# Performance work log

Measured on AMD Instinct MI355X. Metric: run time of the kernel, lower is better.

## Reference

```python
import jax, jax.numpy as jnp
import numpy as np

jax.config.update("jax_enable_x64", True)  # needed for faithful int64 topology hash (31**i weights)

B, SEQ, HID, OUT = 64, 2048, 1024, 1024
MAX_DEPTH = 3
MAX_NODES = 2 ** MAX_DEPTH - 1          # 7
MAX_LEAVES = 2 ** (MAX_DEPTH - 1)       # 4 leaf slots (nodes 3..6)
MAX_SHAPE_IDS = 256


def _gelu(x):
    return jax.nn.gelu(x, approximate=False)  # torch nn.GELU default = exact erf


def setup_inputs() -> dict:
    key = jax.random.key(0)
    ks = jax.random.split(key, 8)
    states = jax.random.normal(ks[0], (B, SEQ, HID), dtype=jnp.float32)

    rng = np.random.default_rng(0)
    lengths = rng.integers(SEQ // 2, SEQ, size=(B,)).astype(np.int64)
    # sorted segment boundaries within [0, lengths), first boundary at 0
    fr = np.sort(rng.random((B, MAX_LEAVES - 1)), axis=1)
    boundaries = np.concatenate(
        [np.zeros((B, 1), np.int64), np.floor(fr * lengths[:, None]).astype(np.int64)], axis=1)
    mask = np.arange(SEQ)[None, :] < lengths[:, None]
    # complete binary tree, depth 3: node 0 root, nodes 1-2 internal, 3-6 leaves
    leaf_order = np.tile(np.arange(MAX_NODES // 2, MAX_NODES, dtype=np.int64), (B, 1))
    active = np.ones((B, MAX_NODES), bool)
    is_leaf = np.concatenate([np.zeros((B, 3), bool), np.ones((B, 4), bool)], axis=1)
    left_child = np.array([1, 3, 5, -1, -1, -1, -1], np.int64)
    right_child = np.array([2, 4, 6, -1, -1, -1, -1], np.int64)
    depth = np.array([0, 1, 1, 2, 2, 2, 2], np.int64)

    def lin(k, fan_in, shape):
        return jax.random.normal(k, shape, dtype=jnp.float32) / np.sqrt(fan_in).astype(np.float32)

    W1 = lin(ks[1], HID, (HID, OUT)); b1 = jnp.zeros((OUT,), jnp.float32)
    W2 = lin(ks[2], OUT, (OUT, OUT)); b2 = jnp.zeros((OUT,), jnp.float32)
    Wm1 = lin(ks[3], 2 * OUT, (2 * OUT, OUT)); bm1 = jnp.zeros((OUT,), jnp.float32)
    Wm2 = lin(ks[4], OUT, (OUT, OUT)); bm2 = jnp.zeros((OUT,), jnp.float32)
    depth_embed = jax.random.normal(ks[5], (MAX_DEPTH, OUT), dtype=jnp.float32) * 0.02
    shape_embed = jax.random.normal(ks[6], (MAX_SHAPE_IDS, OUT), dtype=jnp.float32) * 0.02

    return dict(
        states=states, mask=jnp.asarray(mask), lengths=jnp.asarray(lengths),
        boundaries=jnp.asarray(boundaries), leaf_order=jnp.asarray(leaf_order),
        active=jnp.asarray(active), is_leaf=jnp.asarray(is_leaf),
        left_child=jnp.asarray(left_child), right_child=jnp.asarray(right_child),
        depth=jnp.asarray(depth),
        W1=W1, b1=b1, W2=W2, b2=b2, Wm1=Wm1, bm1=bm1, Wm2=Wm2, bm2=bm2,
        depth_embed=depth_embed, shape_embed=shape_embed)


def _forward(states, W1, b1, W2, b2, Wm1, bm1, Wm2, bm2, depth_embed, shape_embed,
             mask, lengths, boundaries, leaf_order, active, is_leaf,
             left_child, right_child, depth):
    b, seq, _ = states.shape
    S = boundaries.shape[1]
    max_nodes = left_child.shape[0]

    # ---- 1. vectorized ragged masked segment-mean pooling ----
    pos = jnp.arange(seq)
    # segment id per token: number of boundaries <= t, minus 1
    seg_id = (pos[None, None, :] >= boundaries[:, :, None]).sum(1) - 1      # (b, seq)
    valid = mask & (pos[None, :] < lengths[:, None]) & (seg_id >= 0)
    onehot = ((seg_id[:, :, None] == jnp.arange(S)[None, None, :])
              & valid[:, :, None]).astype(states.dtype)                     # (b, seq, S)
    cnt = onehot.sum(1)                                                     # (b, S)
    pooled = jnp.einsum('bts,bth->bsh', onehot, states) / jnp.clip(cnt, 1.0)[..., None]

    # ---- 2. encode segments + depth embedding, scatter to leaf slots ----
    enc = _gelu(pooled @ W1 + b1) @ W2 + b2                                 # (b, S, D)
    nidx = leaf_order                                                       # (b, S)
    nclip = jnp.maximum(nidx, 0)
    enc = enc + depth_embed[depth[nclip]]
    leaf_ok = (nidx >= 0) & jnp.take_along_axis(is_leaf, nclip, axis=1) & (cnt > 0)
    contrib = enc * leaf_ok[..., None].astype(enc.dtype)
    node_repr = jnp.zeros((b, max_nodes, enc.shape[-1]), enc.dtype)
    node_repr = node_repr.at[jnp.arange(b)[:, None], nclip].add(contrib)

    # ---- 3. bottom-up binary tree merge (loop over fixed small node count) ----
    for i in range(max_nodes - 1, -1, -1):
        lc = left_child[i]
        rc = right_child[i]
        is_int = active[:, i] & ~is_leaf[:, i]                              # (b,)
        l = jnp.take(node_repr, jnp.maximum(lc, 0), axis=1)                 # (b, D)
        r = jnp.take(node_repr, jnp.maximum(rc, 0), axis=1)
        merged = (_gelu(jnp.concatenate([l, r], axis=-1) @ Wm1 + bm1) @ Wm2 + bm2
                  + depth_embed[depth[i]])
        upd = is_int.any() & (lc != -1)
        newv = jnp.where(upd, merged * is_int[:, None].astype(merged.dtype),
                         node_repr[:, i])
        node_repr = node_repr.at[:, i].set(newv)

    # ---- 4. topology hash -> shape embedding ----
    pattern = active.astype(jnp.int64) * 2 + is_leaf.astype(jnp.int64)      # (b, nodes)
    weights = 31 ** jnp.arange(max_nodes, dtype=jnp.int64)
    hashed = (pattern * weights[None, :]).sum(1)
    shape_ids = jnp.abs(hashed) % shape_embed.shape[0]
    return node_repr[:, 0] + shape_embed[shape_ids]


def reference(states, mask, lengths, boundaries, leaf_order, active, is_leaf,
              left_child, right_child, depth,
              W1, b1, W2, b2, Wm1, bm1, Wm2, bm2, depth_embed, shape_embed):
    return _forward(states, W1, b1, W2, b2, Wm1, bm1, Wm2, bm2,
                    depth_embed, shape_embed, mask, lengths, boundaries,
                    leaf_order, active, is_leaf, left_child, right_child, depth)
```

## Files before the change

### kernel.cpp

```cpp
#include <hip/hip_runtime.h>
#include <cstdint>
#include <cstddef>

#define SEQ   2048
#define HID   1024
#define NBAT  64
#define NSEG  4
#define NNODE 7
#define TCHUNK 128

__device__ __forceinline__ float gelu_f(float x) {
  return 0.5f * x * (1.0f + erff(x * 0.7071067811865476f));
}

__global__ __launch_bounds__(256) void pool_kernel(
    const float* __restrict__ states, const int* __restrict__ boundaries,
    const int* __restrict__ lengths, float* __restrict__ pooled_sum)
{
  const int tc = blockIdx.x, b = blockIdx.y;
  const int tid = threadIdx.x;
  const int len = lengths[b];
  int bnd[5];
  bnd[0] = boundaries[b * 4 + 0];
  bnd[1] = boundaries[b * 4 + 1];
  bnd[2] = boundaries[b * 4 + 2];
  bnd[3] = boundaries[b * 4 + 3];
  bnd[4] = len;
  const int clo = tc * TCHUNK, chi = clo + TCHUNK;
  const float4* S = (const float4*)(states + (size_t)b * SEQ * HID);

  #pragma unroll
  for (int s = 0; s < NSEG; ++s) {
    int lo = bnd[s]     > clo ? bnd[s]     : clo;
    int hi = bnd[s + 1] < chi ? bnd[s + 1] : chi;
    if (lo >= hi) continue;
    float4 acc = make_float4(0.f, 0.f, 0.f, 0.f);
    int t = lo;
    for (; t + 4 <= hi; t += 4) {
      float4 v0 = S[(size_t)(t + 0) * (HID / 4) + tid];
      float4 v1 = S[(size_t)(t + 1) * (HID / 4) + tid];
      float4 v2 = S[(size_t)(t + 2) * (HID / 4) + tid];
      float4 v3 = S[(size_t)(t + 3) * (HID / 4) + tid];
      acc.x += (v0.x + v1.x) + (v2.x + v3.x);
      acc.y += (v0.y + v1.y) + (v2.y + v3.y);
      acc.z += (v0.z + v1.z) + (v2.z + v3.z);
      acc.w += (v0.w + v1.w) + (v2.w + v3.w);
    }
    for (; t < hi; ++t) {
      float4 v = S[(size_t)t * (HID / 4) + tid];
      acc.x += v.x; acc.y += v.y; acc.z += v.z; acc.w += v.w;
    }
    float* dst = pooled_sum + (size_t)(b * NSEG + s) * HID + tid * 4;
    atomicAdd(dst + 0, acc.x);
    atomicAdd(dst + 1, acc.y);
    atomicAdd(dst + 2, acc.z);
    atomicAdd(dst + 3, acc.w);
  }
}

#define BM 32
#define BN 64
#define BK 32

template<int AMODE, int SPLIT, int SRCS>
__global__ __launch_bounds__(256) void gemm_kernel(
    const float* __restrict__ A,
    const float* __restrict__ W,
    const float* __restrict__ biasA,
    float* __restrict__ Cp,
    int M, int K,
    const int* __restrict__ boundaries, const int* __restrict__ lengths,
    const int* __restrict__ left_child, const int* __restrict__ right_child,
    const float* __restrict__ node_in, int nodeA, int nodeB)
{
  const int N = 1024;
  __shared__ float As[BK][BM + 2];
  __shared__ float Ws[BK][BN];

  const int tid = threadIdx.x;
  const int n0 = blockIdx.x * BN;
  const int m0 = blockIdx.y * BM;
  const int z  = blockIdx.z;
  const int Kloc = K / SPLIT;
  const int kbeg = z * Kloc;

  const int am = tid >> 3;
  const int ak = (tid & 7) * 4;
  const int wk = tid >> 3;
  const int wn = (tid & 7) * 8;
  const int rm = (tid >> 4) * 2;
  const int cn = (tid & 15) * 4;

  float ainv = 1.0f;
  int lcn = 0, rcn = 0, arow_b = 0;
  if constexpr (AMODE == 1) {
    int m = m0 + am; int b = m >> 2; int s = m & 3;
    int bs = boundaries[b * 4 + s];
    int bn = (s < 3) ? boundaries[b * 4 + s + 1] : lengths[b];
    ainv = 1.0f / fmaxf((float)(bn - bs), 1.0f);
  } else if constexpr (AMODE == 2) {
    int mrow = m0 + am; int mi = mrow >> 6; int b = mrow & 63;
    int node = mi ? nodeB : nodeA;
    lcn = left_child[node]; rcn = right_child[node];
    arow_b = b;
  }

  float acc[2][4] = {{0.f,0.f,0.f,0.f},{0.f,0.f,0.f,0.f}};

  float4 av[SRCS]; float4 bv; float4 wv0, wv1;

  auto issueA = [&](int kcol) {
    if constexpr (AMODE == 3) {
      #pragma unroll
      for (int s = 0; s < SRCS; ++s)
        av[s] = *(const float4*)(A + ((size_t)s * M + (m0 + am)) * (size_t)K + kcol);
      bv = *(const float4*)(biasA + kcol);
    } else if constexpr (AMODE == 2) {
      int child = (kcol < 1024) ? lcn : rcn;
      av[0] = *(const float4*)(node_in + (size_t)(arow_b * NNODE + child) * 1024 + (kcol & 1023));
    } else {
      av[0] = *(const float4*)(A + (size_t)(m0 + am) * K + kcol);
    }
  };

  issueA(kbeg + ak);
  wv0 = *(const float4*)(W + (size_t)(kbeg + wk) * N + n0 + wn);
  wv1 = *(const float4*)(W + (size_t)(kbeg + wk) * N + n0 + wn + 4);

  for (int k0 = 0; k0 < Kloc; k0 += BK) {
    __syncthreads();
    {
      float4 a;
      if constexpr (AMODE == 3) {
        float4 s = av[0];
        #pragma unroll
        for (int q = 1; q < SRCS; ++q) {
          s.x += av[q].x; s.y += av[q].y; s.z += av[q].z; s.w += av[q].w;
        }
        a.x = gelu_f(s.x + bv.x); a.y = gelu_f(s.y + bv.y);
        a.z = gelu_f(s.z + bv.z); a.w = gelu_f(s.w + bv.w);
      } else if constexpr (AMODE == 1) {
        a = av[0];
        a.x *= ainv; a.y *= ainv; a.z *= ainv; a.w *= ainv;
      } else {
        a = av[0];
      }
      As[ak + 0][am] = a.x;
      As[ak + 1][am] = a.y;
      As[ak + 2][am] = a.z;
      As[ak + 3][am] = a.w;
    }
    *(float4*)&Ws[wk][wn]     = wv0;
    *(float4*)&Ws[wk][wn + 4] = wv1;
    __syncthreads();

    const int kn = k0 + BK;
    if (kn < Kloc) {
      issueA(kbeg + kn + ak);
      wv0 = *(const float4*)(W + (size_t)(kbeg + kn + wk) * N + n0 + wn);
      wv1 = *(const float4*)(W + (size_t)(kbeg + kn + wk) * N + n0 + wn + 4);
    }

    #pragma unroll
    for (int kk = 0; kk < BK; ++kk) {
      float2 a2 = *(const float2*)&As[kk][rm];
      float4 w  = *(const float4*)&Ws[kk][cn];
      acc[0][0] += a2.x * w.x; acc[0][1] += a2.x * w.y;
      acc[0][2] += a2.x * w.z; acc[0][3] += a2.x * w.w;
      acc[1][0] += a2.y * w.x; acc[1][1] += a2.y * w.y;
      acc[1][2] += a2.y * w.z; acc[1][3] += a2.y * w.w;
    }
  }

  #pragma unroll
  for (int r = 0; r < 2; ++r) {
    const int m = m0 + rm + r;
    *(float4*)(Cp + ((size_t)z * M + m) * N + n0 + cn) =
        make_float4(acc[r][0], acc[r][1], acc[r][2], acc[r][3]);
  }
}

template<int EPI, int SRCS>
__global__ __launch_bounds__(256) void redepi_kernel(
    const float* __restrict__ P, const float* __restrict__ bias, int M,
    const int* __restrict__ boundaries, const int* __restrict__ lengths,
    const int* __restrict__ leaf_order, const int* __restrict__ active,
    const int* __restrict__ is_leaf, const int* __restrict__ depth,
    const float* __restrict__ dembed, const float* __restrict__ sembed,
    float* __restrict__ node_out, int nodeA, int nodeB)
{
  const int m = blockIdx.x;
  const int n = threadIdx.x * 4;

  float4 x = *(const float4*)(P + (size_t)m * 1024 + n);
  #pragma unroll
  for (int q = 1; q < SRCS; ++q) {
    float4 p = *(const float4*)(P + ((size_t)q * M + m) * 1024 + n);
    x.x += p.x; x.y += p.y; x.z += p.z; x.w += p.w;
  }
  x.x += bias[n + 0]; x.y += bias[n + 1];
  x.z += bias[n + 2]; x.w += bias[n + 3];

  if constexpr (EPI == 1) {
    int b = m >> 2; int s = m & 3;
    int node  = leaf_order[b * 4 + s];
    int nclip = node < 0 ? 0 : node;
    int bs = boundaries[b * 4 + s];
    int bn = (s < 3) ? boundaries[b * 4 + s + 1] : lengths[b];
    bool ok = (node >= 0) && (is_leaf[b * NNODE + nclip] != 0) && (bn - bs > 0);
    int d = depth[nclip];
    const float* de = dembed + (size_t)d * 1024 + n;
    float sc = ok ? 1.0f : 0.0f;
    x.x = (x.x + de[0]) * sc; x.y = (x.y + de[1]) * sc;
    x.z = (x.z + de[2]) * sc; x.w = (x.w + de[3]) * sc;
    *(float4*)(node_out + (size_t)(b * NNODE + nclip) * 1024 + n) = x;
  } else if constexpr (EPI == 2) {
    int mi = m >> 6; int b = m & 63;
    int node = mi ? nodeB : nodeA;
    bool ii = (active[b * NNODE + node] != 0) && (is_leaf[b * NNODE + node] == 0);
    int d = depth[node];
    const float* de = dembed + (size_t)d * 1024 + n;
    float sc = ii ? 1.0f : 0.0f;
    x.x = (x.x + de[0]) * sc; x.y = (x.y + de[1]) * sc;
    x.z = (x.z + de[2]) * sc; x.w = (x.w + de[3]) * sc;
    *(float4*)(node_out + (size_t)(b * NNODE + node) * 1024 + n) = x;
  } else {
    int b = m & 63;
    bool ii = (active[b * NNODE + 0] != 0) && (is_leaf[b * NNODE + 0] == 0);
    int d = depth[0];
    const float* de = dembed + (size_t)d * 1024 + n;
    float sc = ii ? 1.0f : 0.0f;
    long long h = 0, w = 1;
    #pragma unroll
    for (int i = 0; i < NNODE; ++i) {
      long long p = (long long)active[b * NNODE + i] * 2
                  + (long long)is_leaf[b * NNODE + i];
      h += p * w;
      w *= 31;
    }
    long long a = h < 0 ? -h : h;
    int sid = (int)(a % 256);
    const float* se = sembed + (size_t)sid * 1024 + n;
    x.x = (x.x + de[0]) * sc + se[0];
    x.y = (x.y + de[1]) * sc + se[1];
    x.z = (x.z + de[2]) * sc + se[2];
    x.w = (x.w + de[3]) * sc + se[3];
    *(float4*)(node_out + (size_t)b * 1024 + n) = x;
  }
}

extern "C" void kernel_launch(void* const* d_in, const int* in_sizes, int n_in,
                              void* d_out, int out_size, void* d_ws, size_t ws_size,
                              hipStream_t stream)
{
  const float* states     = (const float*)d_in[0];
  const int* lengths      = (const int*)d_in[2];
  const int* boundaries   = (const int*)d_in[3];
  const int* leaf_order   = (const int*)d_in[4];
  const int* active       = (const int*)d_in[5];
  const int* is_leaf      = (const int*)d_in[6];
  const int* left_child   = (const int*)d_in[7];
  const int* right_child  = (const int*)d_in[8];
  const int* depth        = (const int*)d_in[9];
  const float* W1  = (const float*)d_in[10];
  const float* b1  = (const float*)d_in[11];
  const float* W2  = (const float*)d_in[12];
  const float* b2  = (const float*)d_in[13];
  const float* Wm1 = (const float*)d_in[14];
  const float* bm1 = (const float*)d_in[15];
  const float* Wm2 = (const float*)d_in[16];
  const float* bm2 = (const float*)d_in[17];
  const float* dembed = (const float*)d_in[18];
  const float* sembed = (const float*)d_in[19];
  float* out = (float*)d_out;

  float* pooled    = (float*)d_ws;
  float* P1 = pooled + 256 * 1024;
  float* P2 = P1 + 2 * 256 * 1024;
  float* P3 = P2 + 2 * 256 * 1024;
  float* P4 = P3 + 4 * 128 * 1024;
  float* P5 = P4 + 4 * 128 * 1024;
  float* P6 = P5 + 8 * 64 * 1024;
  float* node_repr = P6 + 8 * 64 * 1024;

  hipMemsetAsync(pooled, 0, (size_t)256 * 1024 * sizeof(float), stream);

  pool_kernel<<<dim3(SEQ / TCHUNK, NBAT), 256, 0, stream>>>(
      states, boundaries, lengths, pooled);

  gemm_kernel<1, 2, 1><<<dim3(16, 8, 2), 256, 0, stream>>>(
      pooled, W1, nullptr, P1, 256, 1024,
      boundaries, lengths, nullptr, nullptr, nullptr, -1, -1);

  gemm_kernel<3, 2, 2><<<dim3(16, 8, 2), 256, 0, stream>>>(
      P1, W2, b1, P2, 256, 1024,
      nullptr, nullptr, nullptr, nullptr, nullptr, -1, -1);

  redepi_kernel<1, 2><<<dim3(256), 256, 0, stream>>>(
      P2, b2, 256, boundaries, lengths, leaf_order, active, is_leaf, depth,
      dembed, sembed, node_repr, -1, -1);

  gemm_kernel<2, 4, 1><<<dim3(16, 4, 4), 256, 0, stream>>>(
      nullptr, Wm1, nullptr, P3, 128, 2048,
      nullptr, nullptr, left_child, right_child, node_repr, 1, 2);

  gemm_kernel<3, 4, 4><<<dim3(16, 4, 4), 256, 0, stream>>>(
      P3, Wm2, bm1, P4, 128, 1024,
      nullptr, nullptr, nullptr, nullptr, nullptr, -1, -1);

  redepi_kernel<2, 4><<<dim3(128), 256, 0, stream>>>(
      P4, bm2, 128, boundaries, lengths, leaf_order, active, is_leaf, depth,
      dembed, sembed, node_repr, 1, 2);

  gemm_kernel<2, 8, 1><<<dim3(16, 2, 8), 256, 0, stream>>>(
      nullptr, Wm1, nullptr, P5, 64, 2048,
      nullptr, nullptr, left_child, right_child, node_repr, 0, 0);

  gemm_kernel<3, 8, 8><<<dim3(16, 2, 8), 256, 0, stream>>>(
      P5, Wm2, bm1, P6, 64, 1024,
      nullptr, nullptr, nullptr, nullptr, nullptr, -1, -1);

  redepi_kernel<3, 8><<<dim3(64), 256, 0, stream>>>(
      P6, bm2, 64, boundaries, lengths, leaf_order, active, is_leaf, depth,
      dembed, sembed, out, 0, 0);
}
```

Before: 812.2 us.

## Fuse all stages into one persistent kernel with software grid barriers

Replaces the ten separate launches (pool, six split-K GEMMs, three reduce/epilogue kernels) with a single persistent kernel of 512 blocks that separates stages with atomic-counter grid barriers. The split-K reduction, bias and depth-embedding epilogues are folded into the A-operand load of the next GEMM, which removes the node_repr buffer and the redepi kernels. Split factors are doubled to give 512 blocks per stage. The aim is to remove launch gaps and intermediate round trips. The cost is barrier spin overhead and a deadlock risk if all 512 blocks are not co-resident.

```diff
diff --git a/kernel.cpp b/kernel.cpp
--- a/kernel.cpp
+++ b/kernel.cpp
@@ -2,87 +2,103 @@
 #include <cstdint>
 #include <cstddef>
 
-#define SEQ   2048
-#define HID   1024
-#define NBAT  64
-#define NSEG  4
-#define NNODE 7
+#define SEQ    2048
+#define HID    1024
+#define NBAT   64
+#define NSEG   4
+#define NNODE  7
 #define TCHUNK 128
-
-__device__ __forceinline__ float gelu_f(float x) {
-  return 0.5f * x * (1.0f + erff(x * 0.7071067811865476f));
-}
-
-__global__ __launch_bounds__(256) void pool_kernel(
-    const float* __restrict__ states, const int* __restrict__ boundaries,
-    const int* __restrict__ lengths, float* __restrict__ pooled_sum)
-{
-  const int tc = blockIdx.x, b = blockIdx.y;
-  const int tid = threadIdx.x;
-  const int len = lengths[b];
-  int bnd[5];
-  bnd[0] = boundaries[b * 4 + 0];
-  bnd[1] = boundaries[b * 4 + 1];
-  bnd[2] = boundaries[b * 4 + 2];
-  bnd[3] = boundaries[b * 4 + 3];
-  bnd[4] = len;
-  const int clo = tc * TCHUNK, chi = clo + TCHUNK;
-  const float4* S = (const float4*)(states + (size_t)b * SEQ * HID);
-
-  #pragma unroll
-  for (int s = 0; s < NSEG; ++s) {
-    int lo = bnd[s]     > clo ? bnd[s]     : clo;
-    int hi = bnd[s + 1] < chi ? bnd[s + 1] : chi;
-    if (lo >= hi) continue;
-    float4 acc = make_float4(0.f, 0.f, 0.f, 0.f);
-    int t = lo;
-    for (; t + 4 <= hi; t += 4) {
-      float4 v0 = S[(size_t)(t + 0) * (HID / 4) + tid];
-      float4 v1 = S[(size_t)(t + 1) * (HID / 4) + tid];
-      float4 v2 = S[(size_t)(t + 2) * (HID / 4) + tid];
-      float4 v3 = S[(size_t)(t + 3) * (HID / 4) + tid];
-      acc.x += (v0.x + v1.x) + (v2.x + v3.x);
-      acc.y += (v0.y + v1.y) + (v2.y + v3.y);
-      acc.z += (v0.z + v1.z) + (v2.z + v3.z);
-      acc.w += (v0.w + v1.w) + (v2.w + v3.w);
-    }
-    for (; t < hi; ++t) {
-      float4 v = S[(size_t)t * (HID / 4) + tid];
-      acc.x += v.x; acc.y += v.y; acc.z += v.z; acc.w += v.w;
-    }
-    float* dst = pooled_sum + (size_t)(b * NSEG + s) * HID + tid * 4;
-    atomicAdd(dst + 0, acc.x);
-    atomicAdd(dst + 1, acc.y);
-    atomicAdd(dst + 2, acc.z);
-    atomicAdd(dst + 3, acc.w);
-  }
-}
+#define NBLK   512
 
 #define BM 32
 #define BN 64
 #define BK 32
 
-template<int AMODE, int SPLIT, int SRCS>
-__global__ __launch_bounds__(256) void gemm_kernel(
-    const float* __restrict__ A,
-    const float* __restrict__ W,
-    const float* __restrict__ biasA,
-    float* __restrict__ Cp,
-    int M, int K,
+__device__ __forceinline__ float gelu_f(float x) {
+  return 0.5f * x * (1.0f + erff(x * 0.7071067811865476f));
+}
+
+__device__ __forceinline__ void grid_barrier(unsigned* cnt, unsigned target) {
+  __syncthreads();
+  __threadfence();
+  if (threadIdx.x == 0) {
+    __hip_atomic_fetch_add(cnt, 1u, __ATOMIC_RELAXED, __HIP_MEMORY_SCOPE_AGENT);
+    while (__hip_atomic_load(cnt, __ATOMIC_RELAXED, __HIP_MEMORY_SCOPE_AGENT) < target)
+      __builtin_amdgcn_s_sleep(1);
+  }
+  __syncthreads();
+  __threadfence();
+}
+
+__device__ void pool_stage(const float* __restrict__ states,
+                           const int* __restrict__ boundaries,
+                           const int* __restrict__ lengths,
+                           float* __restrict__ pooled_sum) {
+  const int tid = threadIdx.x;
+  for (int task = blockIdx.x; task < 1024; task += NBLK) {
+    const int tc = task & 15, b = task >> 4;
+    const int len = lengths[b];
+    int bnd[5];
+    bnd[0] = boundaries[b * 4 + 0];
+    bnd[1] = boundaries[b * 4 + 1];
+    bnd[2] = boundaries[b * 4 + 2];
+    bnd[3] = boundaries[b * 4 + 3];
+    bnd[4] = len;
+    const int clo = tc * TCHUNK, chi = clo + TCHUNK;
+    const float4* S = (const float4*)(states + (size_t)b * SEQ * HID);
+
+    #pragma unroll
+    for (int s = 0; s < NSEG; ++s) {
+      int lo = bnd[s]     > clo ? bnd[s]     : clo;
+      int hi = bnd[s + 1] < chi ? bnd[s + 1] : chi;
+      if (lo >= hi) continue;
+      float4 acc = make_float4(0.f, 0.f, 0.f, 0.f);
+      int t = lo;
+      for (; t + 4 <= hi; t += 4) {
+        float4 v0 = S[(size_t)(t + 0) * (HID / 4) + tid];
+        float4 v1 = S[(size_t)(t + 1) * (HID / 4) + tid];
+        float4 v2 = S[(size_t)(t + 2) * (HID / 4) + tid];
+        float4 v3 = S[(size_t)(t + 3) * (HID / 4) + tid];
+        acc.x += (v0.x + v1.x) + (v2.x + v3.x);
+        acc.y += (v0.y + v1.y) + (v2.y + v3.y);
+        acc.z += (v0.z + v1.z) + (v2.z + v3.z);
+        acc.w += (v0.w + v1.w) + (v2.w + v3.w);
+      }
+      for (; t < hi; ++t) {
+        float4 v = S[(size_t)t * (HID / 4) + tid];
+        acc.x += v.x; acc.y += v.y; acc.z += v.z; acc.w += v.w;
+      }
+      float* dst = pooled_sum + (size_t)(b * NSEG + s) * HID + tid * 4;
+      atomicAdd(dst + 0, acc.x);
+      atomicAdd(dst + 1, acc.y);
+      atomicAdd(dst + 2, acc.z);
+      atomicAdd(dst + 3, acc.w);
+    }
+  }
+}
+
+template<int AMODE, int SRCS, int NMLOG, int KLOC>
+__device__ void gemm_stage(
+    float (*As)[BM + 2], float (*Ws)[BN],
+    const float* __restrict__ Asrc, const float* __restrict__ W,
+    const float* __restrict__ preb, float* __restrict__ Cp,
+    int prows, int M,
     const int* __restrict__ boundaries, const int* __restrict__ lengths,
+    const int* __restrict__ leaf_order, const int* __restrict__ active,
+    const int* __restrict__ is_leaf, const int* __restrict__ depth,
     const int* __restrict__ left_child, const int* __restrict__ right_child,
-    const float* __restrict__ node_in, int nodeA, int nodeB)
+    const float* __restrict__ dembed, int nodeA, int nodeB)
 {
+  static_assert(KLOC % BK == 0, "KLOC must be a multiple of BK");
   const int N = 1024;
-  __shared__ float As[BK][BM + 2];
-  __shared__ float Ws[BK][BN];
-
   const int tid = threadIdx.x;
-  const int n0 = blockIdx.x * BN;
-  const int m0 = blockIdx.y * BM;
-  const int z  = blockIdx.z;
-  const int Kloc = K / SPLIT;
-  const int kbeg = z * Kloc;
+  const int bid = blockIdx.x;
+  const int nx  = (bid >> 3) & 15;
+  const int g   = (bid & 7) + ((bid >> 7) << 3);
+  const int mi  = g & ((1 << NMLOG) - 1);
+  const int z   = g >> NMLOG;
+  const int n0  = nx * BN, m0 = mi * BM;
+  const int kbeg = z * KLOC;
 
   const int am = tid >> 3;
   const int ak = (tid & 7) * 4;
@@ -91,59 +107,80 @@
   const int rm = (tid >> 4) * 2;
   const int cn = (tid & 15) * 4;
 
-  float ainv = 1.0f;
-  int lcn = 0, rcn = 0, arow_b = 0;
+  float sc = 1.0f;
+  int prow = m0 + am;
+  const float* de = dembed;
   if constexpr (AMODE == 1) {
     int m = m0 + am; int b = m >> 2; int s = m & 3;
-    int bs = boundaries[b * 4 + s];
-    int bn = (s < 3) ? boundaries[b * 4 + s + 1] : lengths[b];
-    ainv = 1.0f / fmaxf((float)(bn - bs), 1.0f);
-  } else if constexpr (AMODE == 2) {
-    int mrow = m0 + am; int mi = mrow >> 6; int b = mrow & 63;
-    int node = mi ? nodeB : nodeA;
-    lcn = left_child[node]; rcn = right_child[node];
-    arow_b = b;
-  }
+    int bs  = boundaries[b * 4 + s];
+    int bn2 = (s < 3) ? boundaries[b * 4 + s + 1] : lengths[b];
+    sc = 1.0f / fmaxf((float)(bn2 - bs), 1.0f);
+  } else if constexpr (AMODE == 4) {
+    int mrow = m0 + am; int nodei = mrow >> 6; int b = mrow & 63;
+    int node = nodei ? nodeB : nodeA;
+    int cd = (kbeg < 1024) ? left_child[node] : right_child[node];
+    int srow = -1;
+    #pragma unroll
+    for (int s = 0; s < 4; ++s)
+      if (leaf_order[b * 4 + s] == cd) srow = s;
+    bool ok = false; prow = 0; int dep = 0;
+    if (cd >= 0 && srow >= 0) {
+      int bs  = boundaries[b * 4 + srow];
+      int bn2 = (srow < 3) ? boundaries[b * 4 + srow + 1] : lengths[b];
+      ok = (is_leaf[b * NNODE + cd] != 0) && (bn2 - bs > 0);
+      prow = b * 4 + srow;
+      dep = depth[cd];
+    }
+    sc = ok ? 1.0f : 0.0f;
+    de = dembed + (size_t)dep * 1024;
+  } else if constexpr (AMODE == 5) {
+    int mrow = m0 + am; int b = mrow & 63;
+    int cd = (kbeg < 1024) ? left_child[nodeA] : right_child[nodeA];
+    prow = 0; int dep = 0; bool ii = false;
+    if (cd >= 1) {
+      ii = (active[b * NNODE + cd] != 0) && (is_leaf[b * NNODE + cd] == 0);
+      prow = (cd - 1) * 64 + b;
+      dep = depth[cd];
+    }
+    sc = ii ? 1.0f : 0.0f;
+    de = dembed + (size_t)dep * 1024;
+  }
+  const int hbase = (AMODE == 4 || AMODE == 5) ? (kbeg & 1023) : kbeg;
 
   float acc[2][4] = {{0.f,0.f,0.f,0.f},{0.f,0.f,0.f,0.f}};
-
-  float4 av[SRCS]; float4 bv; float4 wv0, wv1;
-
-  auto issueA = [&](int kcol) {
-    if constexpr (AMODE == 3) {
-      #pragma unroll
-      for (int s = 0; s < SRCS; ++s)
-        av[s] = *(const float4*)(A + ((size_t)s * M + (m0 + am)) * (size_t)K + kcol);
-      bv = *(const float4*)(biasA + kcol);
-    } else if constexpr (AMODE == 2) {
-      int child = (kcol < 1024) ? lcn : rcn;
-      av[0] = *(const float4*)(node_in + (size_t)(arow_b * NNODE + child) * 1024 + (kcol & 1023));
-    } else {
-      av[0] = *(const float4*)(A + (size_t)(m0 + am) * K + kcol);
-    }
+  float4 av[SRCS], bv, dv, wv0, wv1;
+
+  auto issueA = [&](int koff) {
+    const int h = hbase + koff;
+    #pragma unroll
+    for (int q = 0; q < SRCS; ++q)
+      av[q] = *(const float4*)(Asrc + ((size_t)q * prows + prow) * 1024 + h);
+    if constexpr (AMODE >= 3) bv = *(const float4*)(preb + h);
+    if constexpr (AMODE == 4 || AMODE == 5) dv = *(const float4*)(de + h);
   };
 
-  issueA(kbeg + ak);
+  issueA(ak);
   wv0 = *(const float4*)(W + (size_t)(kbeg + wk) * N + n0 + wn);
   wv1 = *(const float4*)(W + (size_t)(kbeg + wk) * N + n0 + wn + 4);
 
-  for (int k0 = 0; k0 < Kloc; k0 += BK) {
+  #pragma unroll 1
+  for (int k0 = 0; k0 < KLOC; k0 += BK) {
     __syncthreads();
     {
+      float4 s = av[0];
+      #pragma unroll
+      for (int q = 1; q < SRCS; ++q) {
+        s.x += av[q].x; s.y += av[q].y; s.z += av[q].z; s.w += av[q].w;
+      }
       float4 a;
       if constexpr (AMODE == 3) {
-        float4 s = av[0];
-        #pragma unroll
-        for (int q = 1; q < SRCS; ++q) {
-          s.x += av[q].x; s.y += av[q].y; s.z += av[q].z; s.w += av[q].w;
-        }
         a.x = gelu_f(s.x + bv.x); a.y = gelu_f(s.y + bv.y);
         a.z = gelu_f(s.z + bv.z); a.w = gelu_f(s.w + bv.w);
-      } else if constexpr (AMODE == 1) {
-        a = av[0];
-        a.x *= ainv; a.y *= ainv; a.z *= ainv; a.w *= ainv;
+      } else if constexpr (AMODE == 4 || AMODE == 5) {
+        a.x = (s.x + bv.x + dv.x) * sc; a.y = (s.y + bv.y + dv.y) * sc;
+        a.z = (s.z + bv.z + dv.z) * sc; a.w = (s.w + bv.w + dv.w) * sc;
       } else {
-        a = av[0];
+        a.x = s.x * sc; a.y = s.y * sc; a.z = s.z * sc; a.w = s.w * sc;
       }
       As[ak + 0][am] = a.x;
       As[ak + 1][am] = a.y;
@@ -155,8 +192,8 @@
     __syncthreads();
 
     const int kn = k0 + BK;
-    if (kn < Kloc) {
-      issueA(kbeg + kn + ak);
+    if (kn < KLOC) {
+      issueA(kn + ak);
       wv0 = *(const float4*)(W + (size_t)(kbeg + kn + wk) * N + n0 + wn);
       wv1 = *(const float4*)(W + (size_t)(kbeg + kn + wk) * N + n0 + wn + 4);
     }
@@ -175,60 +212,75 @@
   #pragma unroll
   for (int r = 0; r < 2; ++r) {
     const int m = m0 + rm + r;
-    *(float4*)(Cp + ((size_t)z * M + m) * N + n0 + cn) =
+    *(float4*)(Cp + ((size_t)z * M + m) * 1024 + n0 + cn) =
         make_float4(acc[r][0], acc[r][1], acc[r][2], acc[r][3]);
   }
 }
 
-template<int EPI, int SRCS>
-__global__ __launch_bounds__(256) void redepi_kernel(
-    const float* __restrict__ P, const float* __restrict__ bias, int M,
+__global__ __launch_bounds__(256, 2) void fused_kernel(
+    const float* __restrict__ states,
     const int* __restrict__ boundaries, const int* __restrict__ lengths,
     const int* __restrict__ leaf_order, const int* __restrict__ active,
-    const int* __restrict__ is_leaf, const int* __restrict__ depth,
+    const int* __restrict__ is_leaf, const int* __restrict__ left_child,
+    const int* __restrict__ right_child, const int* __restrict__ depth,
+    const float* __restrict__ W1, const float* __restrict__ b1,
+    const float* __restrict__ W2, const float* __restrict__ b2,
+    const float* __restrict__ Wm1, const float* __restrict__ bm1,
+    const float* __restrict__ Wm2, const float* __restrict__ bm2,
     const float* __restrict__ dembed, const float* __restrict__ sembed,
-    float* __restrict__ node_out, int nodeA, int nodeB)
+    float* __restrict__ pooled,
+    float* __restrict__ P1, float* __restrict__ P2, float* __restrict__ P3,
+    float* __restrict__ P4, float* __restrict__ P5, float* __restrict__ P6,
+    unsigned* __restrict__ barcnt, float* __restrict__ out)
 {
-  const int m = blockIdx.x;
-  const int n = threadIdx.x * 4;
-
-  float4 x = *(const float4*)(P + (size_t)m * 1024 + n);
-  #pragma unroll
-  for (int q = 1; q < SRCS; ++q) {
-    float4 p = *(const float4*)(P + ((size_t)q * M + m) * 1024 + n);
-    x.x += p.x; x.y += p.y; x.z += p.z; x.w += p.w;
-  }
-  x.x += bias[n + 0]; x.y += bias[n + 1];
-  x.z += bias[n + 2]; x.w += bias[n + 3];
-
-  if constexpr (EPI == 1) {
-    int b = m >> 2; int s = m & 3;
-    int node  = leaf_order[b * 4 + s];
-    int nclip = node < 0 ? 0 : node;
-    int bs = boundaries[b * 4 + s];
-    int bn = (s < 3) ? boundaries[b * 4 + s + 1] : lengths[b];
-    bool ok = (node >= 0) && (is_leaf[b * NNODE + nclip] != 0) && (bn - bs > 0);
-    int d = depth[nclip];
-    const float* de = dembed + (size_t)d * 1024 + n;
-    float sc = ok ? 1.0f : 0.0f;
-    x.x = (x.x + de[0]) * sc; x.y = (x.y + de[1]) * sc;
-    x.z = (x.z + de[2]) * sc; x.w = (x.w + de[3]) * sc;
-    *(float4*)(node_out + (size_t)(b * NNODE + nclip) * 1024 + n) = x;
-  } else if constexpr (EPI == 2) {
-    int mi = m >> 6; int b = m & 63;
-    int node = mi ? nodeB : nodeA;
-    bool ii = (active[b * NNODE + node] != 0) && (is_leaf[b * NNODE + node] == 0);
-    int d = depth[node];
-    const float* de = dembed + (size_t)d * 1024 + n;
-    float sc = ii ? 1.0f : 0.0f;
-    x.x = (x.x + de[0]) * sc; x.y = (x.y + de[1]) * sc;
-    x.z = (x.z + de[2]) * sc; x.w = (x.w + de[3]) * sc;
-    *(float4*)(node_out + (size_t)(b * NNODE + node) * 1024 + n) = x;
-  } else {
-    int b = m & 63;
+  __shared__ float As[BK][BM + 2];
+  __shared__ float Ws[BK][BN];
+
+  pool_stage(states, boundaries, lengths, pooled);
+  grid_barrier(barcnt, 1 * NBLK);
+
+  gemm_stage<1, 1, 3, 256>(As, Ws, pooled, W1, nullptr, P1, 256, 256,
+      boundaries, lengths, leaf_order, active, is_leaf, depth,
+      left_child, right_child, dembed, -1, -1);
+  grid_barrier(barcnt, 2 * NBLK);
+
+  gemm_stage<3, 4, 3, 256>(As, Ws, P1, W2, b1, P2, 256, 256,
+      boundaries, lengths, leaf_order, active, is_leaf, depth,
+      left_child, right_child, dembed, -1, -1);
+  grid_barrier(barcnt, 3 * NBLK);
+
+  gemm_stage<4, 4, 2, 256>(As, Ws, P2, Wm1, b2, P3, 256, 128,
+      boundaries, lengths, leaf_order, active, is_leaf, depth,
+      left_child, right_child, dembed, 1, 2);
+  grid_barrier(barcnt, 4 * NBLK);
+
+  gemm_stage<3, 8, 2, 128>(As, Ws, P3, Wm2, bm1, P4, 128, 128,
+      boundaries, lengths, leaf_order, active, is_leaf, depth,
+      left_child, right_child, dembed, -1, -1);
+  grid_barrier(barcnt, 5 * NBLK);
+
+  gemm_stage<5, 8, 1, 128>(As, Ws, P4, Wm1, bm2, P5, 128, 64,
+      boundaries, lengths, leaf_order, active, is_leaf, depth,
+      left_child, right_child, dembed, 0, 0);
+  grid_barrier(barcnt, 6 * NBLK);
+
+  gemm_stage<3, 16, 1, 64>(As, Ws, P5, Wm2, bm1, P6, 64, 64,
+      boundaries, lengths, leaf_order, active, is_leaf, depth,
+      left_child, right_child, dembed, -1, -1);
+  grid_barrier(barcnt, 7 * NBLK);
+
+  if (blockIdx.x < 64) {
+    const int b = blockIdx.x;
+    const int n = threadIdx.x * 4;
+    float4 x = *(const float4*)(P6 + (size_t)b * 1024 + n);
+    #pragma unroll
+    for (int q = 1; q < 16; ++q) {
+      float4 p = *(const float4*)(P6 + ((size_t)q * 64 + b) * 1024 + n);
+      x.x += p.x; x.y += p.y; x.z += p.z; x.w += p.w;
+    }
+    x.x += bm2[n + 0]; x.y += bm2[n + 1]; x.z += bm2[n + 2]; x.w += bm2[n + 3];
     bool ii = (active[b * NNODE + 0] != 0) && (is_leaf[b * NNODE + 0] == 0);
-    int d = depth[0];
-    const float* de = dembed + (size_t)d * 1024 + n;
+    const float* de = dembed + (size_t)depth[0] * 1024 + n;
     float sc = ii ? 1.0f : 0.0f;
     long long h = 0, w = 1;
     #pragma unroll
@@ -245,7 +297,7 @@
     x.y = (x.y + de[1]) * sc + se[1];
     x.z = (x.z + de[2]) * sc + se[2];
     x.w = (x.w + de[3]) * sc + se[3];
-    *(float4*)(node_out + (size_t)b * 1024 + n) = x;
+    *(float4*)(out + (size_t)b * 1024 + n) = x;
   }
 }
 
@@ -274,53 +326,20 @@
   const float* sembed = (const float*)d_in[19];
   float* out = (float*)d_out;
 
-  float* pooled    = (float*)d_ws;
+  unsigned* barcnt = (unsigned*)d_ws;
+  float* pooled = (float*)d_ws + 64;
   float* P1 = pooled + 256 * 1024;
-  float* P2 = P1 + 2 * 256 * 1024;
-  float* P3 = P2 + 2 * 256 * 1024;
-  float* P4 = P3 + 4 * 128 * 1024;
-  float* P5 = P4 + 4 * 128 * 1024;
-  float* P6 = P5 + 8 * 64 * 1024;
-  float* node_repr = P6 + 8 * 64 * 1024;
-
-  hipMemsetAsync(pooled, 0, (size_t)256 * 1024 * sizeof(float), stream);
-
-  pool_kernel<<<dim3(SEQ / TCHUNK, NBAT), 256, 0, stream>>>(
-      states, boundaries, lengths, pooled);
-
-  gemm_kernel<1, 2, 1><<<dim3(16, 8, 2), 256, 0, stream>>>(
-      pooled, W1, nullptr, P1, 256, 1024,
-      boundaries, lengths, nullptr, nullptr, nullptr, -1, -1);
-
-  gemm_kernel<3, 2, 2><<<dim3(16, 8, 2), 256, 0, stream>>>(
-      P1, W2, b1, P2, 256, 1024,
-      nullptr, nullptr, nullptr, nullptr, nullptr, -1, -1);
-
-  redepi_kernel<1, 2><<<dim3(256), 256, 0, stream>>>(
-      P2, b2, 256, boundaries, lengths, leaf_order, active, is_leaf, depth,
-      dembed, sembed, node_repr, -1, -1);
-
-  gemm_kernel<2, 4, 1><<<dim3(16, 4, 4), 256, 0, stream>>>(
-      nullptr, Wm1, nullptr, P3, 128, 2048,
-      nullptr, nullptr, left_child, right_child, node_repr, 1, 2);
-
-  gemm_kernel<3, 4, 4><<<dim3(16, 4, 4), 256, 0, stream>>>(
-      P3, Wm2, bm1, P4, 128, 1024,
-      nullptr, nullptr, nullptr, nullptr, nullptr, -1, -1);
-
-  redepi_kernel<2, 4><<<dim3(128), 256, 0, stream>>>(
-      P4, bm2, 128, boundaries, lengths, leaf_order, active, is_leaf, depth,
-      dembed, sembed, node_repr, 1, 2);
-
-  gemm_kernel<2, 8, 1><<<dim3(16, 2, 8), 256, 0, stream>>>(
-      nullptr, Wm1, nullptr, P5, 64, 2048,
-      nullptr, nullptr, left_child, right_child, node_repr, 0, 0);
-
-  gemm_kernel<3, 8, 8><<<dim3(16, 2, 8), 256, 0, stream>>>(
-      P5, Wm2, bm1, P6, 64, 1024,
-      nullptr, nullptr, nullptr, nullptr, nullptr, -1, -1);
-
-  redepi_kernel<3, 8><<<dim3(64), 256, 0, stream>>>(
-      P6, bm2, 64, boundaries, lengths, leaf_order, active, is_leaf, depth,
-      dembed, sembed, out, 0, 0);
-}
+  float* P2 = P1 + 4 * 256 * 1024;
+  float* P3 = P2 + 4 * 256 * 1024;
+  float* P4 = P3 + 8 * 128 * 1024;
+  float* P5 = P4 + 8 * 128 * 1024;
+  float* P6 = P5 + 16 * 64 * 1024;
+
+  hipMemsetAsync(d_ws, 0, (size_t)(64 + 256 * 1024) * sizeof(float), stream);
+
+  fused_kernel<<<dim3(NBLK), dim3(256), 0, stream>>>(
+      states, boundaries, lengths, leaf_order, active, is_leaf,
+      left_child, right_child, depth,
+      W1, b1, W2, b2, Wm1, bm1, Wm2, bm2, dembed, sembed,
+      pooled, P1, P2, P3, P4, P5, P6, barcnt, out);
+}
```

New measurement: 1.536 ms. 1.89x slower.
